# Optimization experiments

Measured on AMD Instinct MI355X. Metric: run time of the kernel, lower is better.

Reference implementation:

```python
import jax, jax.numpy as jnp
from jax import lax
import numpy as np

# Model hyperparameters (match init_kwargs)
Q = 1000          # n_questions
K = 5             # n_categories
D = 1             # n_traits
M = 50            # memory_size
DK = 64           # key_dim
DV = 128          # value_dim
DS = 50           # summary_dim
ABILITY_SCALE = 1.0
B, S = 128, 2048


def setup_inputs() -> dict:
    key = jax.random.key(0)
    ks = jax.random.split(key, 20)
    sd = 0.05
    questions = jax.random.randint(ks[0], (B, S), 0, Q)          # 0 = padding row (zeros)
    responses = jax.random.randint(ks[1], (B, S), 0, K)
    # Embedding tables (padding_idx=0 -> row 0 zeroed, as in nn.Embedding)
    q_embed_w = jax.random.normal(ks[2], (Q + 1, DK), jnp.float32) * sd
    q_embed_w = q_embed_w.at[0].set(0.0)
    item_embed_w = jax.random.normal(ks[3], (Q + 1, DK), jnp.float32) * sd
    item_embed_w = item_embed_w.at[0].set(0.0)
    # value_proj: Linear(key_dim + K, value_dim)
    value_proj_w = jax.random.normal(ks[4], (DK + K, DV), jnp.float32) * sd
    value_proj_b = jnp.zeros((DV,), jnp.float32)
    # DKVMN key memory and learned initial value memory
    key_mem = jax.random.normal(ks[5], (M, DK), jnp.float32) * sd
    init_mem = jax.random.normal(ks[6], (M, DV), jnp.float32) * sd
    # DKVMN write gates: erase (sigmoid) and add (tanh) Linear(value_dim, value_dim)
    erase_w = jax.random.normal(ks[7], (DV, DV), jnp.float32) * sd
    erase_b = jnp.zeros((DV,), jnp.float32)
    add_w = jax.random.normal(ks[8], (DV, DV), jnp.float32) * sd
    add_b = jnp.zeros((DV,), jnp.float32)
    # Summary network: Linear(value_dim + key_dim, summary_dim) + tanh (dropout=0)
    summary_w = jax.random.normal(ks[9], (DV + DK, DS), jnp.float32) * sd
    summary_b = jnp.zeros((DS,), jnp.float32)
    # IRT parameter extractor heads
    theta_w = jax.random.normal(ks[10], (DS, D), jnp.float32) * sd
    theta_b = jnp.zeros((D,), jnp.float32)
    alpha_w = jax.random.normal(ks[11], (DK, D), jnp.float32) * sd
    alpha_b = jnp.zeros((D,), jnp.float32)
    beta_w = jax.random.normal(ks[12], (DK, K - 1), jnp.float32) * sd
    beta_b = jnp.zeros((K - 1,), jnp.float32)
    return dict(questions=questions, responses=responses,
                q_embed_w=q_embed_w, item_embed_w=item_embed_w,
                value_proj_w=value_proj_w, value_proj_b=value_proj_b,
                key_mem=key_mem, init_mem=init_mem,
                erase_w=erase_w, erase_b=erase_b, add_w=add_w, add_b=add_b,
                summary_w=summary_w, summary_b=summary_b,
                theta_w=theta_w, theta_b=theta_b,
                alpha_w=alpha_w, alpha_b=alpha_b,
                beta_w=beta_w, beta_b=beta_b)


def reference(questions, responses, q_embed_w, item_embed_w, value_proj_w, value_proj_b,
              key_mem, init_mem, erase_w, erase_b, add_w, add_b,
              summary_w, summary_b, theta_w, theta_b, alpha_w, alpha_b, beta_w, beta_b):
    Bq, Sq = questions.shape
    # --- Embeddings (fully vectorized over B,S) ---
    q_e = q_embed_w[questions]                     # (B,S,DK) query/key embedding
    item_v = item_embed_w[questions]               # (B,S,DK)
    k_idx = jnp.arange(K, dtype=jnp.float32)       # (K,)
    dist = jnp.abs(k_idx - responses.astype(jnp.float32)[..., None]) / (K - 1)
    resp_feat = jnp.clip(1.0 - dist, 0.0)          # (B,S,K) triangular response feature
    value_embed = jnp.concatenate([item_v, resp_feat], -1) @ value_proj_w + value_proj_b  # (B,S,DV)
    # --- DKVMN attention (does not depend on value memory -> precompute) ---
    attn = jax.nn.softmax(jnp.einsum('bsk,mk->bsm', q_e, key_mem), axis=-1)  # (B,S,M)
    # --- Recurrent read/write over time via scan ---
    mem0 = jnp.broadcast_to(init_mem, (Bq, M, DV))

    def step(mem, inp):
        attn_t, v_t = inp                                   # (B,M), (B,DV)
        read = jnp.einsum('bm,bmv->bv', attn_t, mem)        # read BEFORE write
        erase = jax.nn.sigmoid(v_t @ erase_w + erase_b)     # (B,DV)
        add = jnp.tanh(v_t @ add_w + add_b)                 # (B,DV)
        w = attn_t[:, :, None]                              # (B,M,1)
        mem = mem * (1.0 - w * erase[:, None, :]) + w * add[:, None, :]
        return mem, read

    _, reads = lax.scan(step, mem0,
                        (attn.transpose(1, 0, 2), value_embed.transpose(1, 0, 2)))
    reads = reads.transpose(1, 0, 2)                        # (B,S,DV)
    # --- Summary + IRT heads (vectorized; dropout_rate=0 -> identity) ---
    summary = jnp.tanh(jnp.concatenate([reads, q_e], -1) @ summary_w + summary_b)  # (B,S,DS)
    theta = ABILITY_SCALE * jnp.tanh(summary @ theta_w + theta_b)   # (B,S,D)
    alpha = jax.nn.softplus(q_e @ alpha_w + alpha_b)                # (B,S,D)
    beta = q_e @ beta_w + beta_b                                    # (B,S,K-1)
    # --- GPCM logits: logit_0 = 0, logit_k = sum_{h<=k} (alpha.theta - beta_h) ---
    interaction = jnp.sum(theta * alpha, axis=-1)                   # (B,S)
    steps = interaction[..., None] - beta                           # (B,S,K-1)
    logits = jnp.concatenate(
        [jnp.zeros(steps.shape[:-1] + (1,), steps.dtype), jnp.cumsum(steps, -1)], -1)  # (B,S,K)
    probs = jax.nn.softmax(logits, axis=-1)
    return theta, alpha, beta, logits, probs
```

## Files before the change

### kernel.cpp

```cpp
#include <hip/hip_runtime.h>
#include <hip/hip_bf16.h>

#define BB   128
#define SS   2048
#define NPOS 262144L
#define MM   50
#define DK   64
#define DV   128
#define DS   50
#define KN   5
#define NQ   1000
#define NC   16
#define LC   128

#define ATTNQ_OFF  262144L
#define PREQ_OFF   524288L
#define ALQ_OFF    786432L
#define BQ_OFF     790528L
#define EAQ_OFF    1048576L
#define GIDX_OFF   6168576L
#define READS_OFF  8388608L
#define CC_OFF     75497472L
#define DC_OFF     101711872L
#define WS_NEEDED  127926272L

#define SWo   12160
#define TWo   21810
#define SCo   22180

#define KIDX_NB  1024
#define KQ_NB    4
#define KEAR_NB  2500
#define KFRONT_NB (KIDX_NB + KQ_NB + KEAR_NB)

typedef unsigned short u16;
typedef __attribute__((ext_vector_type(8))) short   short8;
typedef __attribute__((ext_vector_type(4))) float   floatx4;
typedef __attribute__((ext_vector_type(2))) float   float2v;
typedef __attribute__((ext_vector_type(2))) int     int2v;

static __device__ __forceinline__ float b2f(u16 u) {
    union { unsigned int i; float f; } x; x.i = ((unsigned int)u) << 16; return x.f;
}
static __device__ __forceinline__ u16 f2b(float f) {
    union { float f; unsigned int i; } x; x.f = f;
    unsigned int i = x.i;
    return (u16)((i + 0x7fffu + ((i >> 16) & 1u)) >> 16);
}
static __device__ __forceinline__ float fast_tanh(float x) {
    float xc = fminf(15.f, fmaxf(-15.f, x));
    float t = __expf(2.f * xc);
    return (t - 1.f) / (t + 1.f);
}
static __device__ __forceinline__ float2v splat2(float x) {
    return (float2v){x, x};
}
static __device__ __forceinline__ float2v vfma(float2v a, float2v b, float2v c) {
    return __builtin_elementwise_fma(a, b, c);
}
static __device__ __forceinline__ int rfl(int x) {
    return __builtin_amdgcn_readfirstlane(x);
}

__global__ __launch_bounds__(256) void kprep(
    const float* sw, const float* tw, const float* tb, float* wf)
{
    int tid = threadIdx.x;
    for (int i = tid; i < 9600; i += 256) {
        int j = i / 192, k = i - j * 192;
        wf[SWo + i] = sw[k * 50 + j];
    }
    for (int i = tid; i < 50; i += 256) wf[TWo + i] = tw[i];
    if (tid == 0) wf[SCo + 0] = tb[0];
}

__global__ __launch_bounds__(256) void kfront(
    const int* __restrict__ questions, const int* __restrict__ responses,
    const float* __restrict__ qe_w, const float* __restrict__ iv_w,
    const float* __restrict__ vpw, const float* __restrict__ vpb,
    const float* __restrict__ km, const float* __restrict__ sw,
    const float* __restrict__ sb, const float* __restrict__ aw,
    const float* __restrict__ ab, const float* __restrict__ bw,
    const float* __restrict__ bb, const float* __restrict__ ew_,
    const float* __restrict__ adw_, const float* __restrict__ eb,
    const float* __restrict__ adb,
    int2v* __restrict__ gidx, float* __restrict__ attnq,
    float* __restrict__ preq, float* __restrict__ alq,
    float* __restrict__ bq, float* __restrict__ eaq)
{
    int bid = blockIdx.x;
    int tid = threadIdx.x;

    if (bid < KIDX_NB) {
        long pos = (long)bid * 256 + tid;
        int q = questions[pos], r = responses[pos];
        int2v g = { (q * 5 + r) * 256, q * 64 };
        gidx[pos] = g;
        if (pos == NPOS - 1) {
            #pragma unroll
            for (int p = 0; p < 6; ++p) gidx[NPOS + p] = g;
        }
        return;
    }

    if (bid < KIDX_NB + KQ_NB) {
        int q = (bid - KIDX_NB) * 256 + tid;
        if (q >= NQ) return;

        float qe[64];
        const float* qrow = qe_w + (long)q * 64;
        #pragma unroll
        for (int c = 0; c < 16; ++c) {
            floatx4 vv = *(const floatx4*)(qrow + c * 4);
            qe[c*4+0] = vv[0]; qe[c*4+1] = vv[1]; qe[c*4+2] = vv[2]; qe[c*4+3] = vv[3];
        }
        float lg[50];
        #pragma unroll 2
        for (int m = 0; m < 50; ++m) {
            float acc = 0.f;
            #pragma unroll
            for (int k = 0; k < 64; ++k) acc = fmaf(qe[k], km[m * 64 + k], acc);
            lg[m] = acc;
        }
        float mx = -1e30f;
        #pragma unroll
        for (int m = 0; m < 50; ++m) mx = fmaxf(mx, lg[m]);
        float sum = 0.f;
        #pragma unroll
        for (int m = 0; m < 50; ++m) { lg[m] = __expf(lg[m] - mx); sum += lg[m]; }
        float inv = 1.f / sum;
        float* adst = attnq + q * 64;
        #pragma unroll
        for (int m = 0; m < 50; ++m) adst[m] = lg[m] * inv;
        #pragma unroll
        for (int m = 50; m < 64; ++m) adst[m] = 0.f;

        float* pdst = preq + q * 52;
        #pragma unroll 2
        for (int j = 0; j < 50; ++j) {
            float acc = sb[j];
            #pragma unroll
            for (int k = 0; k < 64; ++k)
                acc = fmaf(qe[k], sw[(128 + k) * 50 + j], acc);
            pdst[j] = acc;
        }
        pdst[50] = 0.f; pdst[51] = 0.f;

        float al = ab[0];
        #pragma unroll
        for (int k = 0; k < 64; ++k) al = fmaf(qe[k], aw[k], al);
        alq[q] = (al > 20.f) ? al : log1pf(__expf(al));
        #pragma unroll
        for (int j = 0; j < 4; ++j) {
            float acc = bb[j];
            #pragma unroll
            for (int k = 0; k < 64; ++k) acc = fmaf(qe[k], bw[k * 4 + j], acc);
            bq[q * 4 + j] = acc;
        }
        return;
    }

    {
        __shared__ float vL[2][128];
        int half = tid >> 7;
        int j = tid & 127;
        int qr = (bid - KIDX_NB - KQ_NB) * 2 + half;
        int q = qr / 5, r = qr - q * 5;

        const float* irow = iv_w + (long)q * 64;
        float acc = vpb[j];
        #pragma unroll
        for (int k = 0; k < 64; ++k)
            acc = fmaf(irow[k], vpw[k * 128 + j], acc);
        #pragma unroll
        for (int kk = 0; kk < KN; ++kk) {
            float rf = fmaxf(1.f - fabsf((float)kk - (float)r) * 0.25f, 0.f);
            acc = fmaf(rf, vpw[(64 + kk) * 128 + j], acc);
        }
        vL[half][j] = acc;
        __syncthreads();

        float ea = eb[j], aa = adb[j];
        #pragma unroll
        for (int k = 0; k < 128; ++k) {
            float v = vL[half][k];
            ea = fmaf(v, ew_[k * 128 + j], ea);
            aa = fmaf(v, adw_[k * 128 + j], aa);
        }
        float* dst = eaq + (long)qr * 256;
        dst[2 * j]     = 1.f / (1.f + __expf(-ea));
        dst[2 * j + 1] = fast_tanh(aa);
    }
}

__global__ __launch_bounds__(256) __attribute__((amdgpu_waves_per_eu(5, 8)))
void kp1(
    const int2v* __restrict__ gidx, const float* __restrict__ attnq,
    const float* __restrict__ eaq,
    u16* __restrict__ Cc, u16* __restrict__ Dc)
{
    int b = blockIdx.x & (BB - 1);
    int c = blockIdx.x >> 7;
    int tid = threadIdx.x;
    int v = tid & 127;
    int mh = rfl(tid >> 7);
    int base = mh * 12;
    long tb = (long)b * SS + (long)c * LC;
    const int2v* gx = gidx + tb;

    float2v C[13], D[13];
    #pragma unroll
    for (int i = 0; i < 13; ++i) { C[i] = splat2(1.f); D[i] = splat2(0.f); }

    int eo0 = rfl(gx[0].x), ao0 = rfl(gx[0].y);
    int eo1 = rfl(gx[1].x), ao1 = rfl(gx[1].y);
    int eo2 = rfl(gx[2].x), ao2 = rfl(gx[2].y);
    int eo3 = rfl(gx[3].x), ao3 = rfl(gx[3].y);
    int eo4 = rfl(gx[4].x), ao4 = rfl(gx[4].y);
    int eo5 = rfl(gx[5].x), ao5 = rfl(gx[5].y);
    float2v ea0 = *(const float2v*)(eaq + eo0 + 2 * v);
    float2v ea1 = *(const float2v*)(eaq + eo1 + 2 * v);
    float2v ea2 = *(const float2v*)(eaq + eo2 + 2 * v);
    float2v ea3 = *(const float2v*)(eaq + eo3 + 2 * v);
    float2v wA[13], wB[13];
    {
        const float2v* a0 = (const float2v*)(attnq + ao0) + base;
        const float2v* a1 = (const float2v*)(attnq + ao1) + base;
        #pragma unroll
        for (int i = 0; i < 13; ++i) { wA[i] = a0[i]; wB[i] = a1[i]; }
    }

    for (int t = 0; t < LC; t += 2) {
        float2v ea4 = *(const float2v*)(eaq + eo4 + 2 * v);
        float2v ea5 = *(const float2v*)(eaq + eo5 + 2 * v);
        int2v g6 = gx[t + 6], g7 = gx[t + 7];
        int eo6 = rfl(g6.x), ao6 = rfl(g6.y);
        int eo7 = rfl(g7.x), ao7 = rfl(g7.y);
        const float2v* aw2 = (const float2v*)(attnq + ao2) + base;
        const float2v* aw3 = (const float2v*)(attnq + ao3) + base;
        {
            float2v ne2 = splat2(-ea0.x), a2 = splat2(ea0.y);
            #pragma unroll
            for (int i = 0; i < 13; ++i) {
                float2v tD = vfma(ne2, D[i], a2);
                float2v tC = ne2 * C[i];
                D[i] = vfma(wA[i], tD, D[i]);
                C[i] = vfma(wA[i], tC, C[i]);
            }
        }
        #pragma unroll
        for (int i = 0; i < 13; ++i) wA[i] = aw2[i];
        {
            float2v ne2 = splat2(-ea1.x), a2 = splat2(ea1.y);
            #pragma unroll
            for (int i = 0; i < 13; ++i) {
                float2v tD = vfma(ne2, D[i], a2);
                float2v tC = ne2 * C[i];
                D[i] = vfma(wB[i], tD, D[i]);
                C[i] = vfma(wB[i], tC, C[i]);
            }
        }
        #pragma unroll
        for (int i = 0; i < 13; ++i) wB[i] = aw3[i];
        ea0 = ea2; ea1 = ea3; ea2 = ea4; ea3 = ea5;
        ao2 = ao4; ao3 = ao5;
        eo4 = eo6; eo5 = eo7; ao4 = ao6; ao5 = ao7;
    }

    long o = ((long)(c * BB + b) * 50) * 128 + v;
    #pragma unroll
    for (int i = 0; i < 13; ++i) {
        int ii = base + i;
        Cc[o + (long)(2*ii)   * 128] = f2b(C[i].x);
        Cc[o + (long)(2*ii+1) * 128] = f2b(C[i].y);
        Dc[o + (long)(2*ii)   * 128] = f2b(D[i].x);
        Dc[o + (long)(2*ii+1) * 128] = f2b(D[i].y);
    }
}

__global__ __launch_bounds__(256) void kcomb(
    u16* __restrict__ Cc, const u16* __restrict__ Dc,
    const float* __restrict__ init_mem)
{
    long p = (long)blockIdx.x * 256 + threadIdx.x;
    if (p >= (long)BB * 3200) return;
    int pv = (int)(p % 3200);
    int b  = (int)(p / 3200);
    float2v s = *(const float2v*)(init_mem + 2 * pv);
    long stride = (long)BB * 6400;
    long o = (long)b * 6400 + 2 * pv;

    unsigned int cv[NC], dv[NC];
    #pragma unroll
    for (int c = 0; c < NC; ++c) {
        cv[c] = *(const unsigned int*)(Cc + c * stride + o);
        dv[c] = *(const unsigned int*)(Dc + c * stride + o);
    }
    #pragma unroll
    for (int c = 0; c < NC; ++c) {
        float C0 = b2f((u16)(cv[c] & 0xffffu)), C1 = b2f((u16)(cv[c] >> 16));
        float D0 = b2f((u16)(dv[c] & 0xffffu)), D1 = b2f((u16)(dv[c] >> 16));
        unsigned int sp = (unsigned int)f2b(s.x) | ((unsigned int)f2b(s.y) << 16);
        *(unsigned int*)(Cc + c * stride + o) = sp;
        s.x = fmaf(C0, s.x, D0);
        s.y = fmaf(C1, s.y, D1);
    }
}

__global__ __launch_bounds__(128) __attribute__((amdgpu_waves_per_eu(4, 8)))
void kp2(
    const int2v* __restrict__ gidx, const float* __restrict__ attnq,
    const float* __restrict__ eaq,
    const u16* __restrict__ Sc, u16* __restrict__ ws_reads)
{
    int b = blockIdx.x & (BB - 1);
    int c = blockIdx.x >> 7;
    int v = threadIdx.x;
    long tb = (long)b * SS + (long)c * LC;
    const int2v* gx = gidx + tb;

    float2v M[25];
    {
        long o = ((long)(c * BB + b) * 50) * 128 + v;
        #pragma unroll
        for (int i = 0; i < 25; ++i)
            M[i] = (float2v){ b2f(Sc[o + (long)(2*i) * 128]),
                              b2f(Sc[o + (long)(2*i+1) * 128]) };
    }

    int eo0 = rfl(gx[0].x), ao0 = rfl(gx[0].y);
    int eo1 = rfl(gx[1].x), ao1 = rfl(gx[1].y);
    int eo2 = rfl(gx[2].x), ao2 = rfl(gx[2].y);
    int eo3 = rfl(gx[3].x), ao3 = rfl(gx[3].y);
    int eo4 = rfl(gx[4].x), ao4 = rfl(gx[4].y);
    int eo5 = rfl(gx[5].x), ao5 = rfl(gx[5].y);
    float2v ea0 = *(const float2v*)(eaq + eo0 + 2 * v);
    float2v ea1 = *(const float2v*)(eaq + eo1 + 2 * v);
    float2v ea2 = *(const float2v*)(eaq + eo2 + 2 * v);
    float2v ea3 = *(const float2v*)(eaq + eo3 + 2 * v);
    float2v wA[25], wB[25];
    {
        const float2v* a0 = (const float2v*)(attnq + ao0);
        const float2v* a1 = (const float2v*)(attnq + ao1);
        #pragma unroll
        for (int i = 0; i < 25; ++i) { wA[i] = a0[i]; wB[i] = a1[i]; }
    }

    for (int t = 0; t < LC; t += 2) {
        float2v ea4 = *(const float2v*)(eaq + eo4 + 2 * v);
        float2v ea5 = *(const float2v*)(eaq + eo5 + 2 * v);
        int2v g6 = gx[t + 6], g7 = gx[t + 7];
        int eo6 = rfl(g6.x), ao6 = rfl(g6.y);
        int eo7 = rfl(g7.x), ao7 = rfl(g7.y);
        const float2v* aw2 = (const float2v*)(attnq + ao2);
        const float2v* aw3 = (const float2v*)(attnq + ao3);
        {
            float2v ne2 = splat2(-ea0.x), a2 = splat2(ea0.y);
            float2v r0 = splat2(0.f), r1 = splat2(0.f);
            #pragma unroll
            for (int i = 0; i < 25; ++i) {
                float2v tM = vfma(ne2, M[i], a2);
                if (i & 1) r1 = vfma(wA[i], M[i], r1);
                else       r0 = vfma(wA[i], M[i], r0);
                M[i] = vfma(wA[i], tM, M[i]);
            }
            float2v rs = r0 + r1;
            ws_reads[(tb + t) * 128 + v] = f2b(rs.x + rs.y);
        }
        #pragma unroll
        for (int i = 0; i < 25; ++i) wA[i] = aw2[i];
        {
            float2v ne2 = splat2(-ea1.x), a2 = splat2(ea1.y);
            float2v r0 = splat2(0.f), r1 = splat2(0.f);
            #pragma unroll
            for (int i = 0; i < 25; ++i) {
                float2v tM = vfma(ne2, M[i], a2);
                if (i & 1) r1 = vfma(wB[i], M[i], r1);
                else       r0 = vfma(wB[i], M[i], r0);
                M[i] = vfma(wB[i], tM, M[i]);
            }
            float2v rs = r0 + r1;
            ws_reads[(tb + t + 1) * 128 + v] = f2b(rs.x + rs.y);
        }
        #pragma unroll
        for (int i = 0; i < 25; ++i) wB[i] = aw3[i];
        ea0 = ea2; ea1 = ea3; ea2 = ea4; ea3 = ea5;
        ao2 = ao4; ao3 = ao5;
        eo4 = eo6; eo5 = eo7; ao4 = ao6; ao5 = ao7;
    }
}

__global__ __launch_bounds__(256, 2) void k3(
    const int* __restrict__ questions, const u16* __restrict__ ws_reads,
    const float* __restrict__ wf, const float* __restrict__ preq,
    const float* __restrict__ alq, const float* __restrict__ bq,
    float* __restrict__ out)
{
    __shared__ float stg[2560];
    int tid = threadIdx.x;
    long pos = (long)blockIdx.x * 256 + tid;
    int q = questions[pos];
    const float* swt = wf + SWo;
    const u16* rrow = ws_reads + pos * 128;
    const float* pq = preq + q * 52;

    float2v ch2[64];
    #pragma unroll
    for (int cc = 0; cc < 16; ++cc) {
        short8 vv = *(const short8*)(rrow + cc * 8);
        #pragma unroll
        for (int i = 0; i < 4; ++i)
            ch2[cc*4+i] = (float2v){ b2f((u16)vv[2*i]), b2f((u16)vv[2*i+1]) };
    }

    float dot = 0.f;
    #pragma unroll 2
    for (int j = 0; j < 50; ++j) {
        const float2v* sw2 = (const float2v*)(swt + j * 192);
        float2v a2 = splat2(0.f), a3 = splat2(0.f);
        #pragma unroll
        for (int k = 0; k < 64; k += 2) {
            a2 = vfma(ch2[k],     sw2[k],     a2);
            a3 = vfma(ch2[k + 1], sw2[k + 1], a3);
        }
        float a = pq[j] + a2.x + a2.y + a3.x + a3.y;
        dot = fmaf(fast_tanh(a), wf[TWo + j], dot);
    }
    float theta = fast_tanh(dot + wf[SCo + 0]);
    float alpha = alq[q];
    floatx4 bet = *(const floatx4*)(bq + q * 4);

    float inter = theta * alpha;
    float l1 = inter - bet[0];
    float l2 = l1 + inter - bet[1];
    float l3 = l2 + inter - bet[2];
    float l4 = l3 + inter - bet[3];
    float mx = fmaxf(0.f, fmaxf(fmaxf(l1, l2), fmaxf(l3, l4)));
    float e0 = __expf(0.f - mx), e1 = __expf(l1 - mx), e2 = __expf(l2 - mx);
    float e3 = __expf(l3 - mx), e4 = __expf(l4 - mx);
    float inv = 1.f / (e0 + e1 + e2 + e3 + e4);

    out[pos] = theta;
    out[NPOS + pos] = alpha;
    *(floatx4*)(out + 2L * NPOS + pos * 4) = bet;

    stg[tid * 5 + 0] = 0.f;
    stg[tid * 5 + 1] = l1;  stg[tid * 5 + 2] = l2;
    stg[tid * 5 + 3] = l3;  stg[tid * 5 + 4] = l4;
    stg[1280 + tid * 5 + 0] = e0 * inv;
    stg[1280 + tid * 5 + 1] = e1 * inv;
    stg[1280 + tid * 5 + 2] = e2 * inv;
    stg[1280 + tid * 5 + 3] = e3 * inv;
    stg[1280 + tid * 5 + 4] = e4 * inv;
    __syncthreads();
    float* ol = out + 6L * NPOS + (long)blockIdx.x * 1280;
    float* op = out + 11L * NPOS + (long)blockIdx.x * 1280;
    #pragma unroll
    for (int i = 0; i < 5; ++i) {
        ol[i * 256 + tid] = stg[i * 256 + tid];
        op[i * 256 + tid] = stg[1280 + i * 256 + tid];
    }
}

extern "C" void kernel_launch(void* const* d_in, const int* in_sizes, int n_in,
                              void* d_out, int out_size, void* d_ws, size_t ws_size,
                              hipStream_t stream)
{
    if (ws_size < (size_t)WS_NEEDED) return;

    const int*   questions = (const int*)d_in[0];
    const int*   responses = (const int*)d_in[1];
    const float* qe_w      = (const float*)d_in[2];
    const float* iv_w      = (const float*)d_in[3];
    const float* vp_w      = (const float*)d_in[4];
    const float* vp_b      = (const float*)d_in[5];
    const float* key_mem   = (const float*)d_in[6];
    const float* init_mem  = (const float*)d_in[7];
    const float* erase_w   = (const float*)d_in[8];
    const float* erase_b   = (const float*)d_in[9];
    const float* add_w     = (const float*)d_in[10];
    const float* add_b     = (const float*)d_in[11];
    const float* summary_w = (const float*)d_in[12];
    const float* summary_b = (const float*)d_in[13];
    const float* theta_w   = (const float*)d_in[14];
    const float* theta_b   = (const float*)d_in[15];
    const float* alpha_w   = (const float*)d_in[16];
    const float* alpha_b   = (const float*)d_in[17];
    const float* beta_w    = (const float*)d_in[18];
    const float* beta_b    = (const float*)d_in[19];

    char* ws = (char*)d_ws;
    float* wf    = (float*)ws;
    float* attnq = (float*)(ws + ATTNQ_OFF);
    float* preq  = (float*)(ws + PREQ_OFF);
    float* alq   = (float*)(ws + ALQ_OFF);
    float* bq    = (float*)(ws + BQ_OFF);
    float* eaq   = (float*)(ws + EAQ_OFF);
    int2v* gidx  = (int2v*)(ws + GIDX_OFF);
    u16*   ws_reads = (u16*)(ws + READS_OFF);
    u16*   Cc    = (u16*)(ws + CC_OFF);
    u16*   Dc    = (u16*)(ws + DC_OFF);
    float* out   = (float*)d_out;

    hipLaunchKernelGGL(kfront, dim3(KFRONT_NB), dim3(256), 0, stream,
        questions, responses, qe_w, iv_w, vp_w, vp_b, key_mem, summary_w,
        summary_b, alpha_w, alpha_b, beta_w, beta_b, erase_w, add_w,
        erase_b, add_b, gidx, attnq, preq, alq, bq, eaq);
    hipLaunchKernelGGL(kprep, dim3(1), dim3(256), 0, stream,
        summary_w, theta_w, theta_b, wf);
    hipLaunchKernelGGL(kp1, dim3((NC - 1) * BB), dim3(256), 0, stream,
        gidx, attnq, eaq, Cc, Dc);
    hipLaunchKernelGGL(kcomb, dim3(1600), dim3(256), 0, stream,
        Cc, Dc, init_mem);
    hipLaunchKernelGGL(kp2, dim3(NC * BB), dim3(128), 0, stream,
        gidx, attnq, eaq, Cc, ws_reads);
    hipLaunchKernelGGL(k3, dim3(1024), dim3(256), 0, stream,
        questions, ws_reads, wf, preq, alq, bq, out);
}
```

Baseline: 526.8 us.

## Fuse output head into scan kernel and fold weight prep into front kernel

The summary/IRT head kernel k3 is merged into the tail of the chunked scan kernel kp2, so each 128-position chunk computes its outputs right after writing its reads. The kprep weight-transpose kernel becomes an extra block of kfront. This removes two kernel launches and their inter-kernel gaps, and the head now reads reads that were just written and may still be in cache. In exchange, kp2f carries more registers and shared memory, which is why its waves-per-EU hint is lowered and occupancy may drop.

```diff
diff --git a/kernel.cpp b/kernel.cpp
--- a/kernel.cpp
+++ b/kernel.cpp
@@ -31,7 +31,8 @@
 #define KIDX_NB  1024
 #define KQ_NB    4
 #define KEAR_NB  2500
-#define KFRONT_NB (KIDX_NB + KQ_NB + KEAR_NB)
+#define KPREP_NB 1
+#define KFRONT_NB (KIDX_NB + KQ_NB + KEAR_NB + KPREP_NB)
 
 typedef unsigned short u16;
 typedef __attribute__((ext_vector_type(8))) short   short8;
@@ -60,18 +61,6 @@
 }
 static __device__ __forceinline__ int rfl(int x) {
     return __builtin_amdgcn_readfirstlane(x);
-}
-
-__global__ __launch_bounds__(256) void kprep(
-    const float* sw, const float* tw, const float* tb, float* wf)
-{
-    int tid = threadIdx.x;
-    for (int i = tid; i < 9600; i += 256) {
-        int j = i / 192, k = i - j * 192;
-        wf[SWo + i] = sw[k * 50 + j];
-    }
-    for (int i = tid; i < 50; i += 256) wf[TWo + i] = tw[i];
-    if (tid == 0) wf[SCo + 0] = tb[0];
 }
 
 __global__ __launch_bounds__(256) void kfront(
@@ -83,10 +72,12 @@
     const float* __restrict__ ab, const float* __restrict__ bw,
     const float* __restrict__ bb, const float* __restrict__ ew_,
     const float* __restrict__ adw_, const float* __restrict__ eb,
-    const float* __restrict__ adb,
+    const float* __restrict__ adb, const float* __restrict__ tw,
+    const float* __restrict__ tb,
     int2v* __restrict__ gidx, float* __restrict__ attnq,
     float* __restrict__ preq, float* __restrict__ alq,
-    float* __restrict__ bq, float* __restrict__ eaq)
+    float* __restrict__ bq, float* __restrict__ eaq,
+    float* __restrict__ wf)
 {
     int bid = blockIdx.x;
     int tid = threadIdx.x;
@@ -160,7 +151,7 @@
         return;
     }
 
-    {
+    if (bid < KIDX_NB + KQ_NB + KEAR_NB) {
         __shared__ float vL[2][128];
         int half = tid >> 7;
         int j = tid & 127;
@@ -190,6 +181,16 @@
         float* dst = eaq + (long)qr * 256;
         dst[2 * j]     = 1.f / (1.f + __expf(-ea));
         dst[2 * j + 1] = fast_tanh(aa);
+        return;
+    }
+
+    {
+        for (int i = tid; i < 9600; i += 256) {
+            int j = i / 192, k = i - j * 192;
+            wf[SWo + i] = sw[k * 50 + j];
+        }
+        for (int i = tid; i < 50; i += 256) wf[TWo + i] = tw[i];
+        if (tid == 0) wf[SCo + 0] = tb[0];
     }
 }
 
@@ -307,12 +308,16 @@
     }
 }
 
-__global__ __launch_bounds__(128) __attribute__((amdgpu_waves_per_eu(4, 8)))
-void kp2(
+__global__ __launch_bounds__(128) __attribute__((amdgpu_waves_per_eu(3, 8)))
+void kp2f(
     const int2v* __restrict__ gidx, const float* __restrict__ attnq,
     const float* __restrict__ eaq,
-    const u16* __restrict__ Sc, u16* __restrict__ ws_reads)
+    const u16* __restrict__ Sc, u16* __restrict__ ws_reads,
+    const int* __restrict__ questions, const float* __restrict__ wf,
+    const float* __restrict__ preq, const float* __restrict__ alq,
+    const float* __restrict__ bq, float* __restrict__ out)
 {
+    __shared__ float stg[1280];
     int b = blockIdx.x & (BB - 1);
     int c = blockIdx.x >> 7;
     int v = threadIdx.x;
@@ -388,17 +393,11 @@
         ao2 = ao4; ao3 = ao5;
         eo4 = eo6; eo5 = eo7; ao4 = ao6; ao5 = ao7;
     }
-}
-
-__global__ __launch_bounds__(256, 2) void k3(
-    const int* __restrict__ questions, const u16* __restrict__ ws_reads,
-    const float* __restrict__ wf, const float* __restrict__ preq,
-    const float* __restrict__ alq, const float* __restrict__ bq,
-    float* __restrict__ out)
-{
-    __shared__ float stg[2560];
-    int tid = threadIdx.x;
-    long pos = (long)blockIdx.x * 256 + tid;
+
+    __threadfence_block();
+    __syncthreads();
+
+    long pos = tb + v;
     int q = questions[pos];
     const float* swt = wf + SWo;
     const u16* rrow = ws_reads + pos * 128;
@@ -444,21 +443,21 @@
     out[NPOS + pos] = alpha;
     *(floatx4*)(out + 2L * NPOS + pos * 4) = bet;
 
-    stg[tid * 5 + 0] = 0.f;
-    stg[tid * 5 + 1] = l1;  stg[tid * 5 + 2] = l2;
-    stg[tid * 5 + 3] = l3;  stg[tid * 5 + 4] = l4;
-    stg[1280 + tid * 5 + 0] = e0 * inv;
-    stg[1280 + tid * 5 + 1] = e1 * inv;
-    stg[1280 + tid * 5 + 2] = e2 * inv;
-    stg[1280 + tid * 5 + 3] = e3 * inv;
-    stg[1280 + tid * 5 + 4] = e4 * inv;
+    stg[v * 5 + 0] = 0.f;
+    stg[v * 5 + 1] = l1;  stg[v * 5 + 2] = l2;
+    stg[v * 5 + 3] = l3;  stg[v * 5 + 4] = l4;
+    stg[640 + v * 5 + 0] = e0 * inv;
+    stg[640 + v * 5 + 1] = e1 * inv;
+    stg[640 + v * 5 + 2] = e2 * inv;
+    stg[640 + v * 5 + 3] = e3 * inv;
+    stg[640 + v * 5 + 4] = e4 * inv;
     __syncthreads();
-    float* ol = out + 6L * NPOS + (long)blockIdx.x * 1280;
-    float* op = out + 11L * NPOS + (long)blockIdx.x * 1280;
+    float* ol = out + 6L * NPOS + tb * 5;
+    float* op = out + 11L * NPOS + tb * 5;
     #pragma unroll
     for (int i = 0; i < 5; ++i) {
-        ol[i * 256 + tid] = stg[i * 256 + tid];
-        op[i * 256 + tid] = stg[1280 + i * 256 + tid];
+        ol[i * 128 + v] = stg[i * 128 + v];
+        op[i * 128 + v] = stg[640 + i * 128 + v];
     }
 }
 
@@ -505,15 +504,13 @@
     hipLaunchKernelGGL(kfront, dim3(KFRONT_NB), dim3(256), 0, stream,
         questions, responses, qe_w, iv_w, vp_w, vp_b, key_mem, summary_w,
         summary_b, alpha_w, alpha_b, beta_w, beta_b, erase_w, add_w,
-        erase_b, add_b, gidx, attnq, preq, alq, bq, eaq);
-    hipLaunchKernelGGL(kprep, dim3(1), dim3(256), 0, stream,
-        summary_w, theta_w, theta_b, wf);
+        erase_b, add_b, theta_w, theta_b,
+        gidx, attnq, preq, alq, bq, eaq, wf);
     hipLaunchKernelGGL(kp1, dim3((NC - 1) * BB), dim3(256), 0, stream,
         gidx, attnq, eaq, Cc, Dc);
     hipLaunchKernelGGL(kcomb, dim3(1600), dim3(256), 0, stream,
         Cc, Dc, init_mem);
-    hipLaunchKernelGGL(kp2, dim3(NC * BB), dim3(128), 0, stream,
-        gidx, attnq, eaq, Cc, ws_reads);
-    hipLaunchKernelGGL(k3, dim3(1024), dim3(256), 0, stream,
-        questions, ws_reads, wf, preq, alq, bq, out);
-}
+    hipLaunchKernelGGL(kp2f, dim3(NC * BB), dim3(128), 0, stream,
+        gidx, attnq, eaq, Cc, ws_reads,
+        questions, wf, preq, alq, bq, out);
+}
```

New measurement: 501.6 us. -4.8%, faster.
